# Performance work log

Hardware: AMD Instinct MI355X
Metric: run time of the kernel (lower is better)

Reference implementation:

```python
import jax, jax.numpy as jnp
import numpy as np

B, D, G, L = 8, 128, 2048, 24
GF = G // 2 + 1  # rfft bins
EPS = 1e-5


def setup_inputs() -> dict:
    key = jax.random.key(0)
    ks = jax.random.split(key, 6)
    x = jax.random.normal(ks[0], (B, D, G), dtype=jnp.float32)
    Phi_f = jax.random.normal(ks[1], (L, GF), dtype=jnp.float32) * 0.1
    Theta = jax.random.normal(ks[2], (L, D, D), dtype=jnp.float32) * (1.0 / np.sqrt(D))
    ln_gamma = jnp.ones((D,), dtype=jnp.float32)
    ln_beta = jnp.zeros((D,), dtype=jnp.float32)
    fc1_w = jax.random.normal(ks[3], (2 * D, D), dtype=jnp.float32) * (1.0 / np.sqrt(D))
    fc1_b = jnp.zeros((2 * D,), dtype=jnp.float32)
    fc2_w = jax.random.normal(ks[4], (D, 2 * D), dtype=jnp.float32) * (1.0 / np.sqrt(2 * D))
    fc2_b = jnp.zeros((D,), dtype=jnp.float32)
    return {
        'x': x, 'Phi_f': Phi_f, 'Theta': Theta,
        'ln_gamma': ln_gamma, 'ln_beta': ln_beta,
        'fc1_w': fc1_w, 'fc1_b': fc1_b, 'fc2_w': fc2_w, 'fc2_b': fc2_b,
    }


def reference(x, Phi_f, Theta, ln_gamma, ln_beta, fc1_w, fc1_b, fc2_w, fc2_b):
    # x: (B, D, G). LayerNorm over the lifting (channel) dim D.
    mean = jnp.mean(x, axis=1, keepdims=True)
    var = jnp.var(x, axis=1, keepdims=True)
    z = (x - mean) * jax.lax.rsqrt(var + EPS)
    z = z * ln_gamma[None, :, None] + ln_beta[None, :, None]

    # Spectral convolution with each Hilbert filter.
    Xf = jnp.fft.rfft(z, axis=-1)                       # (B, D, GF) complex
    Uf = Xf[:, :, None, :] * jnp.conj(Phi_f)[None, None]  # (B, D, L, GF)
    U = jnp.fft.irfft(Uf, n=G, axis=-1)                 # (B, D, L, G)

    # Per-filter channel mixing then reduction over filters:
    # einsum('bdln,lhd->bhln') followed by sum over l, fused:
    S = jnp.einsum('bdlg,lhd->bhg', U, Theta)           # (B, D, G)

    # Pointwise MLP (Conv1d kernel_size=1 == channel matmul).
    H = jnp.einsum('hd,bdg->bhg', fc1_w, S) + fc1_b[None, :, None]
    H = jax.nn.gelu(H, approximate=False)
    out = jnp.einsum('dh,bhg->bdg', fc2_w, H) + fc2_b[None, :, None]
    return x + out
```

## Files before the change

### kernel.cpp

```cpp
#include <hip/hip_runtime.h>
#include <math.h>


#define B_   8
#define D_   128
#define G_   2048
#define L_   24
#define GF_  1025
#define BD_  1024
#define DD_  16384
#define GH_  1024
#define CF_  1026
#define MF_  1088
#define NF_  2048

#define PA_CV0 64
#define PA_TT0 130
#define PA_WF0 386
#define PA_WI0 1474
#define PA_END 2498

#define G1_NB  544
#define G1_END 4768

typedef __attribute__((ext_vector_type(8))) short  short8v;
typedef __attribute__((ext_vector_type(4))) float  float4v;

union FU { float f; unsigned int u; };
union V8 { short8v v; ushort u[8]; };
union V4 { uint2 p; ushort u[4]; };

static __device__ __forceinline__ float bf2f(ushort h) {
    FU v; v.u = ((unsigned int)h) << 16; return v.f;
}
static __device__ __forceinline__ ushort f2bf(float f) {
    FU v; v.f = f;
    unsigned int r = v.u + 0x7fffu + ((v.u >> 16) & 1u);
    return (ushort)(r >> 16);
}
static __device__ __forceinline__ void async16(const void* g, void* l) {
    __builtin_amdgcn_global_load_lds(
        (const __attribute__((address_space(1))) void*)g,
        (__attribute__((address_space(3))) void*)l, 16, 0, 0);
}
static __device__ __forceinline__ int is_f32(const unsigned int* graw) {
    return graw[0] == 0x3F800000u;
}

__global__ __launch_bounds__(256) void k_pre(
        const void* __restrict__ x_raw,  const void* __restrict__ th_raw,
        const unsigned int* __restrict__ graw, const void* __restrict__ be_raw,
        const void* __restrict__ w1_raw, const void* __restrict__ b1_raw,
        const void* __restrict__ w2_raw, const void* __restrict__ b2_raw,
        ushort* __restrict__ z,  ushort* __restrict__ wf,
        ushort* __restrict__ wi, ushort* __restrict__ thT,
        ushort* __restrict__ w1c, ushort* __restrict__ b1c,
        ushort* __restrict__ w2c, ushort* __restrict__ b2c) {
    __shared__ ushort T[L_][72];
    int bid = blockIdx.x, tid = threadIdx.x;

    if (bid < PA_CV0) {
        int fl = is_f32(graw);
        int b  = bid >> 3;
        int g  = (bid & 7) * 256 + tid;
        float s = 0.f, ss = 0.f;
        if (fl) {
            const float* xp = (const float*)x_raw + (size_t)b * D_ * G_ + g;
            for (int d = 0; d < D_; ++d) {
                float v = xp[(size_t)d * G_];
                s += v; ss += v * v;
            }
        } else {
            const ushort* xp = (const ushort*)x_raw + (size_t)b * D_ * G_ + g;
            for (int d = 0; d < D_; ++d) {
                float v = bf2f(xp[(size_t)d * G_]);
                s += v; ss += v * v;
            }
        }
        float mean = s * (1.f / D_);
        float var  = ss * (1.f / D_) - mean * mean;
        float inv  = rsqrtf(var + 1e-5f);
        ushort* zp = z + (size_t)(g & 1) * (BD_ * GH_) +
                     (size_t)(b * D_) * GH_ + (g >> 1);
        if (fl) {
            const float* xp = (const float*)x_raw + (size_t)b * D_ * G_ + g;
            const float* gp = (const float*)graw;
            const float* bp = (const float*)be_raw;
            for (int d = 0; d < D_; ++d) {
                float o = (xp[(size_t)d * G_] - mean) * inv * gp[d] + bp[d];
                zp[(size_t)d * GH_] = f2bf(o);
            }
        } else {
            const ushort* xp = (const ushort*)x_raw + (size_t)b * D_ * G_ + g;
            const ushort* gp = (const ushort*)graw;
            const ushort* bp = (const ushort*)be_raw;
            for (int d = 0; d < D_; ++d) {
                float o = (bf2f(xp[(size_t)d * G_]) - mean) * inv * bf2f(gp[d])
                        + bf2f(bp[d]);
                zp[(size_t)d * GH_] = f2bf(o);
            }
        }
    } else if (bid < PA_TT0) {
        int fl = is_f32(graw);
        int lb = bid - PA_CV0;
        const void* src; ushort* dst; int n, rel;
        if (lb < 32)       { src = w1_raw; dst = w1c; n = 32768; rel = lb; }
        else if (lb == 32) { src = b1_raw; dst = b1c; n = 256;   rel = 0; }
        else if (lb < 65)  { src = w2_raw; dst = w2c; n = 32768; rel = lb - 33; }
        else               { src = b2_raw; dst = b2c; n = 128;   rel = 0; }
        int i0 = rel * 1024 + tid * 4;
        if (fl) {
            const float* s = (const float*)src;
            #pragma unroll
            for (int j = 0; j < 4; ++j) {
                int k = i0 + j;
                if (k < n) dst[k] = f2bf(s[k]);
            }
        } else {
            const ushort* s = (const ushort*)src;
            #pragma unroll
            for (int j = 0; j < 4; ++j) {
                int k = i0 + j;
                if (k < n) dst[k] = s[k];
            }
        }
    } else if (bid < PA_WF0) {
        int fl = is_f32(graw);
        int hd0 = (bid - PA_TT0) * 64;
        if (tid < 192) {
            int l = tid >> 3, c8 = tid & 7;
            V8 o;
            if (fl) {
                const float* tp = (const float*)th_raw + (size_t)l * DD_ +
                                  hd0 + c8 * 8;
                float4v a0 = *(const float4v*)tp;
                float4v a1 = *(const float4v*)(tp + 4);
                #pragma unroll
                for (int j = 0; j < 4; ++j) {
                    o.u[j] = f2bf(a0[j]); o.u[4 + j] = f2bf(a1[j]);
                }
            } else {
                o.v = *(const short8v*)((const ushort*)th_raw +
                                        (size_t)l * DD_ + hd0 + c8 * 8);
            }
            *(short8v*)&T[l][c8 * 8] = o.v;
        }
        __syncthreads();
        int hdl = tid & 63, part = tid >> 6;
        V8 o;
        #pragma unroll
        for (int j = 0; j < 8; ++j) {
            int l = part * 8 + j;
            o.u[j] = (l < L_) ? T[l][hdl] : (ushort)0;
        }
        *(short8v*)(thT + (size_t)(hd0 + hdl) * 32 + part * 8) = o.v;
    } else if (bid < PA_WI0) {
        int c  = bid - PA_WF0;
        int g0 = tid * 4;
        V4 v;
        if (c >= CF_) {
            #pragma unroll
            for (int j = 0; j < 4; ++j) v.u[j] = 0;
        } else {
            int f = c >> 1, im = c & 1;
            #pragma unroll
            for (int j = 0; j < 4; ++j) {
                int g = g0 + j;
                int r = (f * g) & (GH_ - 1);
                float th = (float)r * 6.135923151542565e-3f;
                v.u[j] = f2bf(im ? -__sinf(th) : __cosf(th));
            }
        }
        *(uint2*)(wf + (size_t)c * GH_ + g0) = v.p;
    } else {
        int g = bid - PA_WI0;
        for (int ch = tid; ch < MF_ / 8; ch += 256) {
            int c0 = ch * 8;
            V8 v;
            #pragma unroll
            for (int j = 0; j < 8; ++j) {
                int c = c0 + j;
                if (c >= CF_) { v.u[j] = 0; continue; }
                int f = c >> 1, im = c & 1;
                float a = (f == 0 || f == GH_ / 2) ? (1.f / 2048.f)
                                                   : (1.f / 1024.f);
                int r = (f * g) & (GH_ - 1);
                float th = (float)r * 6.135923151542565e-3f;
                v.u[j] = f2bf(im ? -a * __sinf(th) : a * __cosf(th));
            }
            *(short8v*)(wi + (size_t)g * MF_ + c0) = v.v;
        }
    }
}

__global__ __launch_bounds__(256, 4) void k_g1(
        const ushort* __restrict__ wf, const ushort* __restrict__ z,
        float* __restrict__ zft,
        const void* __restrict__ phi_raw, const unsigned int* __restrict__ graw,
        const ushort* __restrict__ thT, ushort* __restrict__ M) {
    __shared__ ushort As[2][64 * 64];
    __shared__ ushort Bs[2][64 * 64];
    __shared__ ushort Aph[16][40];
    int bid = blockIdx.x, tid = threadIdx.x;
    int w = tid >> 6, lane = tid & 63;
    int lr = lane & 15, q = lane >> 4;

    if (bid < G1_NB) {
        int m0 = (bid >> 5) * 64;
        int n0 = (bid & 31) * 64;
        int wm = (w & 1) * 32, wn = (w >> 1) * 32;
        int rl = lane >> 3, c8 = (lane & 7) ^ rl;
        int t0 = w * 2, t1 = w * 2 + 1;
        const ushort* gA0 = wf + (size_t)(m0 + t0 * 8 + rl) * GH_ + c8 * 8;
        const ushort* gA1 = wf + (size_t)(m0 + t1 * 8 + rl) * GH_ + c8 * 8;
        const ushort* gB0 = z  + (size_t)(n0 + t0 * 8 + rl) * GH_ + c8 * 8;
        const ushort* gB1 = z  + (size_t)(n0 + t1 * 8 + rl) * GH_ + c8 * 8;

        float4v acc00 = {0.f,0.f,0.f,0.f}, acc01 = {0.f,0.f,0.f,0.f};
        float4v acc10 = {0.f,0.f,0.f,0.f}, acc11 = {0.f,0.f,0.f,0.f};

        async16(gA0, &As[0][t0 * 512]);
        async16(gA1, &As[0][t1 * 512]);
        async16(gB0, &Bs[0][t0 * 512]);
        async16(gB1, &Bs[0][t1 * 512]);
        __syncthreads();

        int buf = 0;
        for (int k0 = 0; k0 < GH_; k0 += 64) {
            if (k0 + 64 < GH_) {
                int nb = buf ^ 1;
                async16(gA0 + k0 + 64, &As[nb][t0 * 512]);
                async16(gA1 + k0 + 64, &As[nb][t1 * 512]);
                async16(gB0 + k0 + 64, &Bs[nb][t0 * 512]);
                async16(gB1 + k0 + 64, &Bs[nb][t1 * 512]);
            }
            const ushort* Ab = &As[buf][0];
            const ushort* Bb = &Bs[buf][0];
            #pragma unroll
            for (int s = 0; s < 2; ++s) {
                int cs = s * 4 + q;
                int ra0 = wm + lr, ra1 = wm + 16 + lr;
                int rb0 = wn + lr, rb1 = wn + 16 + lr;
                short8v a0 = *(const short8v*)(Ab + ra0 * 64 + ((cs ^ (ra0 & 7)) << 3));
                short8v a1 = *(const short8v*)(Ab + ra1 * 64 + ((cs ^ (ra1 & 7)) << 3));
                short8v b0 = *(const short8v*)(Bb + rb0 * 64 + ((cs ^ (rb0 & 7)) << 3));
                short8v b1 = *(const short8v*)(Bb + rb1 * 64 + ((cs ^ (rb1 & 7)) << 3));
                acc00 = __builtin_amdgcn_mfma_f32_16x16x32_bf16(a0, b0, acc00, 0, 0, 0);
                acc01 = __builtin_amdgcn_mfma_f32_16x16x32_bf16(a0, b1, acc01, 0, 0, 0);
                acc10 = __builtin_amdgcn_mfma_f32_16x16x32_bf16(a1, b0, acc10, 0, 0, 0);
                acc11 = __builtin_amdgcn_mfma_f32_16x16x32_bf16(a1, b1, acc11, 0, 0, 0);
            }
            __syncthreads();
            buf ^= 1;
        }

        float4v accs[2][2] = { { acc00, acc01 }, { acc10, acc11 } };
        #pragma unroll
        for (int i = 0; i < 2; ++i)
            #pragma unroll
            for (int j = 0; j < 2; ++j) {
                int col = n0 + wn + j * 16 + lr;
                int row = m0 + wm + i * 16 + q * 4;
                #pragma unroll
                for (int r = 0; r < 4; ++r)
                    zft[(size_t)(row + r) * NF_ + col] = accs[i][j][r];
            }
    } else {
        int bb  = bid - G1_NB;
        int f0  = (bb >> 6) * 16;
        int hd0 = (bb & 63) * 256;
        int isf = is_f32(graw);
        #pragma unroll
        for (int rep = 0; rep < 2; ++rep) {
            int idx = rep * 256 + tid;
            int fl = idx >> 5, l = idx & 31;
            int f = f0 + fl;
            ushort v = 0;
            if (l < L_ && f < GF_)
                v = isf ? f2bf(((const float*)phi_raw)[(size_t)l * GF_ + f])
                        : ((const ushort*)phi_raw)[(size_t)l * GF_ + f];
            Aph[fl][l] = v;
        }
        __syncthreads();
        short8v a = *(const short8v*)&Aph[lr][q * 8];
        #pragma unroll
        for (int t = 0; t < 4; ++t) {
            int n = hd0 + (w * 4 + t) * 16 + lr;
            short8v b = *(const short8v*)(thT + (size_t)n * 32 + q * 8);
            float4v c = {0.f, 0.f, 0.f, 0.f};
            c = __builtin_amdgcn_mfma_f32_16x16x32_bf16(a, b, c, 0, 0, 0);
            #pragma unroll
            for (int r = 0; r < 4; ++r) {
                int f = f0 + q * 4 + r;
                if (f < GF_) M[(size_t)f * DD_ + n] = f2bf(c[r]);
            }
        }
    }
}

__global__ __launch_bounds__(256, 2) void k_mix3(const float* __restrict__ zft,
                                                 const ushort* __restrict__ M,
                                                 ushort* __restrict__ sft) {
    int fp  = blockIdx.x;
    int fb  = GH_ - fp;
    int tid = threadIdx.x;
    int w = tid >> 6, lane = tid & 63;
    int lr = lane & 15, q = lane >> 4;
    int cc = lr >> 3, bb = lr & 7;

    float ang = (float)fp * 3.0679615757712823e-3f;
    float wr  = cosf(ang), sn = sinf(ang);
    float wi_ = -sn;
    float wsig = cc ? wi_ : -wi_;
    float cbv  = cc ? wr  : -wr;
    float asgn = cc ? -1.f : 1.f;

    const float* rc = zft + (size_t)(2 * fp + cc) * NF_;
    const float* ro = zft + (size_t)(2 * fp + (cc ^ 1)) * NF_;
    int colb = bb * 128 + q * 8;

    short8v aZ[4], aZb[4];
    #pragma unroll
    for (int s = 0; s < 4; ++s) {
        int col = colb + s * 32;
        float4v av0 = *(const float4v*)(rc + col);
        float4v av1 = *(const float4v*)(rc + col + 4);
        float4v bv0 = *(const float4v*)(rc + BD_ + col);
        float4v bv1 = *(const float4v*)(rc + BD_ + col + 4);
        float4v bo0 = *(const float4v*)(ro + BD_ + col);
        float4v bo1 = *(const float4v*)(ro + BD_ + col + 4);
        V8 tz, tb;
        #pragma unroll
        for (int j = 0; j < 4; ++j) {
            float av = av0[j], bv = bv0[j], bo = bo0[j];
            float zz = fmaf(wsig, bo, fmaf(wr, bv, av));
            float zb = fmaf(cbv, bv, fmaf(wi_, bo, asgn * av));
            tz.u[j] = f2bf(zz); tb.u[j] = f2bf(zb);
            av = av1[j]; bv = bv1[j]; bo = bo1[j];
            zz = fmaf(wsig, bo, fmaf(wr, bv, av));
            zb = fmaf(cbv, bv, fmaf(wi_, bo, asgn * av));
            tz.u[4 + j] = f2bf(zz); tb.u[4 + j] = f2bf(zb);
        }
        aZ[s] = tz.v; aZb[s] = tb.v;
    }

    const ushort* Mf = M + (size_t)fp * DD_;
    const ushort* Mb = M + (size_t)fb * DD_;
    #pragma unroll
    for (int n = 0; n < 2; ++n) {
        int nt = 2 * w + n;
        float4v c1 = {0.f, 0.f, 0.f, 0.f};
        float4v c2 = {0.f, 0.f, 0.f, 0.f};
        #pragma unroll
        for (int s = 0; s < 4; ++s) {
            short8v b1 = *(const short8v*)(Mf + (size_t)(nt * 16 + lr) * D_ +
                                           s * 32 + q * 8);
            short8v b2 = *(const short8v*)(Mb + (size_t)(nt * 16 + lr) * D_ +
                                           s * 32 + q * 8);
            c1 = __builtin_amdgcn_mfma_f32_16x16x32_bf16(aZ[s],  b1, c1, 0, 0, 0);
            c2 = __builtin_amdgcn_mfma_f32_16x16x32_bf16(aZb[s], b2, c2, 0, 0, 0);
        }
        #pragma unroll
        for (int r = 0; r < 4; ++r) {
            int p   = q * 4 + r;
            int c2i = p >> 3, b2 = p & 7;
            float sgm = c2i ? -1.f : 1.f;
            float se  = c1[r] + sgm * c2[r];
            float sop = c1[r] - sgm * c2[r];
            float pp  = __shfl_xor(sop, 32);
            float tsg = c2i ? sn : -sn;
            float so  = fmaf(tsg, pp, sop * wr);
            size_t rowo = (size_t)(2 * fp + c2i) * NF_;
            int colh = b2 * 128 + nt * 16 + lr;
            sft[rowo + colh]       = f2bf(se);
            sft[rowo + BD_ + colh] = f2bf(so);
        }
    }
}

__global__ __launch_bounds__(256, 4) void k_gemm64t(const ushort* __restrict__ A,
                                                    const ushort* __restrict__ Bm,
                                                    float* __restrict__ C,
                                                    int K, int lda, int ldb,
                                                    int ldc, int kv) {
    __shared__ ushort As[2][64 * 64];
    __shared__ ushort Bs[2][64 * 64];
    int tid = threadIdx.x;
    int m0 = blockIdx.x * 64, n0 = blockIdx.y * 64;
    int w = tid >> 6, lane = tid & 63;
    int lr = lane & 15, q = lane >> 4;
    int wm = (w & 1) * 32, wn = (w >> 1) * 32;

    int rl = lane >> 3, c8 = (lane & 7) ^ rl;
    int t0 = w * 2, t1 = w * 2 + 1;
    const ushort* gA0 = A + (size_t)(m0 + t0 * 8 + rl) * lda + c8 * 8;
    const ushort* gA1 = A + (size_t)(m0 + t1 * 8 + rl) * lda + c8 * 8;

    int br = tid >> 2;
    int bc = tid & 3;

    float4v acc00 = {0.f,0.f,0.f,0.f}, acc01 = {0.f,0.f,0.f,0.f};
    float4v acc10 = {0.f,0.f,0.f,0.f}, acc11 = {0.f,0.f,0.f,0.f};

    async16(gA0, &As[0][t0 * 512]);
    async16(gA1, &As[0][t1 * 512]);
    {
        V8 u0, u1;
        if (br < kv) {
            const ushort* gb = Bm + (size_t)br * ldb + n0 + bc * 16;
            u0.v = *(const short8v*)gb;
            u1.v = *(const short8v*)(gb + 8);
        } else {
            #pragma unroll
            for (int j = 0; j < 8; ++j) { u0.u[j] = 0; u1.u[j] = 0; }
        }
        #pragma unroll
        for (int j = 0; j < 8; ++j) {
            int n = bc * 16 + j;
            Bs[0][n * 64 + ((((br >> 3) ^ (n & 7)) << 3) | (br & 7))] = u0.u[j];
        }
        #pragma unroll
        for (int j = 0; j < 8; ++j) {
            int n = bc * 16 + 8 + j;
            Bs[0][n * 64 + ((((br >> 3) ^ (n & 7)) << 3) | (br & 7))] = u1.u[j];
        }
    }
    __syncthreads();

    int buf = 0;
    for (int k0 = 0; k0 < K; k0 += 64) {
        V8 u0, u1;
        bool more = (k0 + 64 < K);
        if (more) {
            int nb = buf ^ 1;
            async16(gA0 + k0 + 64, &As[nb][t0 * 512]);
            async16(gA1 + k0 + 64, &As[nb][t1 * 512]);
            int kr = k0 + 64 + br;
            if (kr < kv) {
                const ushort* gb = Bm + (size_t)kr * ldb + n0 + bc * 16;
                u0.v = *(const short8v*)gb;
                u1.v = *(const short8v*)(gb + 8);
            } else {
                #pragma unroll
                for (int j = 0; j < 8; ++j) { u0.u[j] = 0; u1.u[j] = 0; }
            }
        }
        const ushort* Ab = &As[buf][0];
        const ushort* Bb = &Bs[buf][0];
        #pragma unroll
        for (int s = 0; s < 2; ++s) {
            int cs = s * 4 + q;
            int ra0 = wm + lr, ra1 = wm + 16 + lr;
            int rb0 = wn + lr, rb1 = wn + 16 + lr;
            short8v a0 = *(const short8v*)(Ab + ra0 * 64 + ((cs ^ (ra0 & 7)) << 3));
            short8v a1 = *(const short8v*)(Ab + ra1 * 64 + ((cs ^ (ra1 & 7)) << 3));
            short8v b0 = *(const short8v*)(Bb + rb0 * 64 + ((cs ^ (rb0 & 7)) << 3));
            short8v b1 = *(const short8v*)(Bb + rb1 * 64 + ((cs ^ (rb1 & 7)) << 3));
            acc00 = __builtin_amdgcn_mfma_f32_16x16x32_bf16(a0, b0, acc00, 0, 0, 0);
            acc01 = __builtin_amdgcn_mfma_f32_16x16x32_bf16(a0, b1, acc01, 0, 0, 0);
            acc10 = __builtin_amdgcn_mfma_f32_16x16x32_bf16(a1, b0, acc10, 0, 0, 0);
            acc11 = __builtin_amdgcn_mfma_f32_16x16x32_bf16(a1, b1, acc11, 0, 0, 0);
        }
        __syncthreads();
        if (more) {
            int nb = buf ^ 1;
            #pragma unroll
            for (int j = 0; j < 8; ++j) {
                int n = bc * 16 + j;
                Bs[nb][n * 64 + ((((br >> 3) ^ (n & 7)) << 3) | (br & 7))] = u0.u[j];
            }
            #pragma unroll
            for (int j = 0; j < 8; ++j) {
                int n = bc * 16 + 8 + j;
                Bs[nb][n * 64 + ((((br >> 3) ^ (n & 7)) << 3) | (br & 7))] = u1.u[j];
            }
        }
        __syncthreads();
        buf ^= 1;
    }

    float4v accs[2][2] = { { acc00, acc01 }, { acc10, acc11 } };
    #pragma unroll
    for (int i = 0; i < 2; ++i)
        #pragma unroll
        for (int j = 0; j < 2; ++j) {
            int col = n0 + wn + j * 16 + lr;
            int row = m0 + wm + i * 16 + q * 4;
            #pragma unroll
            for (int r = 0; r < 4; ++r)
                C[(size_t)(row + r) * ldc + col] = accs[i][j][r];
        }
}

#define MLPG 32
__global__ __launch_bounds__(256, 2) void k_mlp3(const float* __restrict__ ST,
                                                 const void* __restrict__ x0,
                                                 const ushort* __restrict__ w1,
                                                 const ushort* __restrict__ b1,
                                                 const ushort* __restrict__ w2,
                                                 const ushort* __restrict__ b2,
                                                 const unsigned int* __restrict__ graw,
                                                 void* __restrict__ outv) {
    __shared__ ushort Sb[MLPG][136];
    __shared__ ushort Hb[MLPG][264];
    __shared__ float  Ob[128][36];
    int g0 = blockIdx.x * MLPG, b = blockIdx.y;
    int tid = threadIdx.x;
    {
        int col = tid >> 3, seg = tid & 7;
        int g = g0 + col;
        const float* sp = ST + (size_t)(g >> 1) * NF_ + (g & 1) * BD_ +
                          b * D_ + seg * 16;
        float4v v0 = *(const float4v*)(sp);
        float4v v1 = *(const float4v*)(sp + 4);
        float4v v2 = *(const float4v*)(sp + 8);
        float4v v3 = *(const float4v*)(sp + 12);
        V8 o0, o1;
        #pragma unroll
        for (int k = 0; k < 4; ++k) { o0.u[k] = f2bf(v0[k]); o0.u[4 + k] = f2bf(v1[k]); }
        #pragma unroll
        for (int k = 0; k < 4; ++k) { o1.u[k] = f2bf(v2[k]); o1.u[4 + k] = f2bf(v3[k]); }
        *(short8v*)&Sb[col][seg * 16]     = o0.v;
        *(short8v*)&Sb[col][seg * 16 + 8] = o1.v;
    }
    __syncthreads();
    int w = tid >> 6, lane = tid & 63;
    int lr = lane & 15, q = lane >> 4;
    int nt = w & 1, mh = w >> 1;

    {
        float4v acc[8];
        #pragma unroll
        for (int i = 0; i < 8; ++i) { float4v zz = {0.f,0.f,0.f,0.f}; acc[i] = zz; }
        #pragma unroll
        for (int ks = 0; ks < 4; ++ks) {
            short8v bf = *(const short8v*)&Sb[nt * 16 + lr][ks * 32 + q * 8];
            #pragma unroll
            for (int i = 0; i < 8; ++i) {
                int mt = mh * 8 + i;
                short8v af = *(const short8v*)(w1 + (size_t)(mt * 16 + lr) * D_ +
                                               ks * 32 + q * 8);
                acc[i] = __builtin_amdgcn_mfma_f32_16x16x32_bf16(af, bf, acc[i], 0, 0, 0);
            }
        }
        #pragma unroll
        for (int i = 0; i < 8; ++i) {
            int h0 = (mh * 8 + i) * 16 + q * 4;
            V4 hv;
            #pragma unroll
            for (int r = 0; r < 4; ++r) {
                float v = acc[i][r] + bf2f(b1[h0 + r]);
                v = 0.5f * v * (1.f + erff(v * 0.70710678118f));
                hv.u[r] = f2bf(v);
            }
            *(uint2*)&Hb[nt * 16 + lr][h0] = hv.p;
        }
    }
    __syncthreads();
    {
        float4v acc2[4];
        #pragma unroll
        for (int j = 0; j < 4; ++j) { float4v zz = {0.f,0.f,0.f,0.f}; acc2[j] = zz; }
        #pragma unroll
        for (int ks = 0; ks < 8; ++ks) {
            short8v bf = *(const short8v*)&Hb[nt * 16 + lr][ks * 32 + q * 8];
            #pragma unroll
            for (int j = 0; j < 4; ++j) {
                int mt2 = mh * 4 + j;
                short8v af = *(const short8v*)(w2 + (size_t)(mt2 * 16 + lr) * (2 * D_) +
                                               ks * 32 + q * 8);
                acc2[j] = __builtin_amdgcn_mfma_f32_16x16x32_bf16(af, bf, acc2[j], 0, 0, 0);
            }
        }
        int col = nt * 16 + lr;
        #pragma unroll
        for (int j = 0; j < 4; ++j) {
            int d0 = (mh * 4 + j) * 16 + q * 4;
            #pragma unroll
            for (int r = 0; r < 4; ++r)
                Ob[d0 + r][col] = acc2[j][r] + bf2f(b2[d0 + r]);
        }
    }
    __syncthreads();
    {
        int fl = is_f32(graw);
        if (fl) {
            #pragma unroll
            for (int p = 0; p < 4; ++p) {
                int idx = p * 256 + tid;
                int d = idx >> 3, c4 = (idx & 7) * 4;
                float4v o = *(const float4v*)&Ob[d][c4];
                size_t gidx = ((size_t)(b * D_ + d)) * G_ + g0 + c4;
                float4v xv = *(const float4v*)((const float*)x0 + gidx);
                float4v ov;
                #pragma unroll
                for (int k = 0; k < 4; ++k) ov[k] = o[k] + xv[k];
                *(float4v*)((float*)outv + gidx) = ov;
            }
        } else {
            #pragma unroll
            for (int p = 0; p < 4; ++p) {
                int idx = p * 256 + tid;
                int d = idx >> 3, c4 = (idx & 7) * 4;
                float4v o = *(const float4v*)&Ob[d][c4];
                size_t gidx = ((size_t)(b * D_ + d)) * G_ + g0 + c4;
                V4 xv; xv.p = *(const uint2*)((const ushort*)x0 + gidx);
                V4 ov;
                #pragma unroll
                for (int k = 0; k < 4; ++k) ov.u[k] = f2bf(o[k] + bf2f(xv.u[k]));
                *(uint2*)((ushort*)outv + gidx) = ov.p;
            }
        }
    }
}

extern "C" void kernel_launch(void* const* d_in, const int* in_sizes, int n_in,
                              void* d_out, int out_size, void* d_ws, size_t ws_size,
                              hipStream_t stream) {
    char* base = (char*)d_ws;
    ushort* z    = (ushort*)(base);
    ushort* wf   = (ushort*)(base + 4194304);
    ushort* sft  = (ushort*)(base);
    float*  zft  = (float*)(base + 13107200);
    float*  st   = (float*)(base + 13107200);
    ushort* w1c  = (ushort*)(base + 27050048);
    ushort* b1c  = (ushort*)(base + 27115584);
    ushort* w2c  = (ushort*)(base + 27116096);
    ushort* b2c  = (ushort*)(base + 27181632);
    ushort* Mm   = (ushort*)(base + 27182592);
    ushort* wi   = (ushort*)(base + 60769792);
    ushort* thT  = (ushort*)(base + 69420544);

    const unsigned int* graw = (const unsigned int*)d_in[3];

    k_pre    <<<dim3(PA_END), 256, 0, stream>>>(
        d_in[0], d_in[2], graw, d_in[4], d_in[5], d_in[6], d_in[7], d_in[8],
        z, wf, wi, thT, w1c, b1c, w2c, b2c);
    k_g1     <<<dim3(G1_END), 256, 0, stream>>>(wf, z, zft, d_in[1], graw,
                                                thT, Mm);
    k_mix3   <<<dim3(513), 256, 0, stream>>>(zft, Mm, sft);
    k_gemm64t<<<dim3(GH_ / 64, NF_ / 64), 256, 0, stream>>>(
        wi, sft, st, MF_, MF_, NF_, NF_, CF_);
    k_mlp3   <<<dim3(G_ / MLPG, B_), 256, 0, stream>>>(st, d_in[0], w1c, b1c,
                                                       w2c, b2c, graw, d_out);
}
```

Baseline: 168.8 us.

## Widen forward-DFT GEMM tile, split LayerNorm over channels, emit bf16 spectral output

The forward DFT GEMM in k_g1 moves from 64x64 to 128x64 tiles, with each wave computing a 64x32 sub-tile. This raises MFMA work per LDS B-fragment load and cuts the block count. The M dimension is padded to 1152 rows, with launch bounds reduced to 3 waves per SIMD. The LayerNorm pre-pass now splits each column's 128 channels across four waves, reduces the statistics in LDS and keeps x in registers, so there are more blocks and no second global read of x. The inverse-DFT GEMM writes bf16 instead of fp32 and the MLP reads it directly, halving that intermediate's traffic at a small precision cost.

```diff
diff --git a/kernel.cpp b/kernel.cpp
--- a/kernel.cpp
+++ b/kernel.cpp
@@ -12,16 +12,17 @@
 #define GH_  1024
 #define CF_  1026
 #define MF_  1088
+#define MFW_ 1152
 #define NF_  2048
 
-#define PA_CV0 64
-#define PA_TT0 130
-#define PA_WF0 386
-#define PA_WI0 1474
-#define PA_END 2498
-
-#define G1_NB  544
-#define G1_END 4768
+#define PA_CV0 256
+#define PA_TT0 322
+#define PA_WF0 578
+#define PA_WI0 1730
+#define PA_END 2754
+
+#define G1_NB  288
+#define G1_END 4512
 
 typedef __attribute__((ext_vector_type(8))) short  short8v;
 typedef __attribute__((ext_vector_type(4))) float  float4v;
@@ -57,46 +58,64 @@
         ushort* __restrict__ w1c, ushort* __restrict__ b1c,
         ushort* __restrict__ w2c, ushort* __restrict__ b2c) {
     __shared__ ushort T[L_][72];
+    __shared__ float red[2][256];
+    __shared__ float mi[2][64];
     int bid = blockIdx.x, tid = threadIdx.x;
 
     if (bid < PA_CV0) {
         int fl = is_f32(graw);
-        int b  = bid >> 3;
-        int g  = (bid & 7) * 256 + tid;
+        int b  = bid >> 5;
+        int g0 = (bid & 31) * 64;
+        int gi = tid & 63, dq = tid >> 6;
+        int g  = g0 + gi;
+        int d0 = dq * 32;
+        float vals[32];
         float s = 0.f, ss = 0.f;
         if (fl) {
-            const float* xp = (const float*)x_raw + (size_t)b * D_ * G_ + g;
-            for (int d = 0; d < D_; ++d) {
+            const float* xp = (const float*)x_raw + (size_t)(b * D_ + d0) * G_ + g;
+            #pragma unroll 8
+            for (int d = 0; d < 32; ++d) {
                 float v = xp[(size_t)d * G_];
-                s += v; ss += v * v;
+                vals[d] = v; s += v; ss += v * v;
             }
         } else {
-            const ushort* xp = (const ushort*)x_raw + (size_t)b * D_ * G_ + g;
-            for (int d = 0; d < D_; ++d) {
+            const ushort* xp = (const ushort*)x_raw + (size_t)(b * D_ + d0) * G_ + g;
+            #pragma unroll 8
+            for (int d = 0; d < 32; ++d) {
                 float v = bf2f(xp[(size_t)d * G_]);
-                s += v; ss += v * v;
-            }
-        }
-        float mean = s * (1.f / D_);
-        float var  = ss * (1.f / D_) - mean * mean;
-        float inv  = rsqrtf(var + 1e-5f);
+                vals[d] = v; s += v; ss += v * v;
+            }
+        }
+        red[0][tid] = s; red[1][tid] = ss;
+        __syncthreads();
+        if (tid < 64) {
+            float S  = red[0][tid] + red[0][tid + 64] + red[0][tid + 128] +
+                       red[0][tid + 192];
+            float SS = red[1][tid] + red[1][tid + 64] + red[1][tid + 128] +
+                       red[1][tid + 192];
+            float mean = S * (1.f / D_);
+            float var  = SS * (1.f / D_) - mean * mean;
+            mi[0][tid] = mean;
+            mi[1][tid] = rsqrtf(var + 1e-5f);
+        }
+        __syncthreads();
+        float mean = mi[0][gi], inv = mi[1][gi];
         ushort* zp = z + (size_t)(g & 1) * (BD_ * GH_) +
-                     (size_t)(b * D_) * GH_ + (g >> 1);
+                     (size_t)(b * D_ + d0) * GH_ + (g >> 1);
         if (fl) {
-            const float* xp = (const float*)x_raw + (size_t)b * D_ * G_ + g;
-            const float* gp = (const float*)graw;
-            const float* bp = (const float*)be_raw;
-            for (int d = 0; d < D_; ++d) {
-                float o = (xp[(size_t)d * G_] - mean) * inv * gp[d] + bp[d];
+            const float* gp = (const float*)graw + d0;
+            const float* bp = (const float*)be_raw + d0;
+            #pragma unroll 8
+            for (int d = 0; d < 32; ++d) {
+                float o = (vals[d] - mean) * inv * gp[d] + bp[d];
                 zp[(size_t)d * GH_] = f2bf(o);
             }
         } else {
-            const ushort* xp = (const ushort*)x_raw + (size_t)b * D_ * G_ + g;
-            const ushort* gp = (const ushort*)graw;
-            const ushort* bp = (const ushort*)be_raw;
-            for (int d = 0; d < D_; ++d) {
-                float o = (bf2f(xp[(size_t)d * G_]) - mean) * inv * bf2f(gp[d])
-                        + bf2f(bp[d]);
+            const ushort* gp = (const ushort*)graw + d0;
+            const ushort* bp = (const ushort*)be_raw + d0;
+            #pragma unroll 8
+            for (int d = 0; d < 32; ++d) {
+                float o = (vals[d] - mean) * inv * bf2f(gp[d]) + bf2f(bp[d]);
                 zp[(size_t)d * GH_] = f2bf(o);
             }
         }
@@ -193,12 +212,12 @@
     }
 }
 
-__global__ __launch_bounds__(256, 4) void k_g1(
+__global__ __launch_bounds__(256, 3) void k_g1(
         const ushort* __restrict__ wf, const ushort* __restrict__ z,
         float* __restrict__ zft,
         const void* __restrict__ phi_raw, const unsigned int* __restrict__ graw,
         const ushort* __restrict__ thT, ushort* __restrict__ M) {
-    __shared__ ushort As[2][64 * 64];
+    __shared__ ushort As[2][128 * 64];
     __shared__ ushort Bs[2][64 * 64];
     __shared__ ushort Aph[16][40];
     int bid = blockIdx.x, tid = threadIdx.x;
@@ -206,64 +225,74 @@
     int lr = lane & 15, q = lane >> 4;
 
     if (bid < G1_NB) {
-        int m0 = (bid >> 5) * 64;
+        int m0 = (bid >> 5) * 128;
         int n0 = (bid & 31) * 64;
-        int wm = (w & 1) * 32, wn = (w >> 1) * 32;
+        int wm = (w & 1) * 64, wn = (w >> 1) * 32;
         int rl = lane >> 3, c8 = (lane & 7) ^ rl;
-        int t0 = w * 2, t1 = w * 2 + 1;
-        const ushort* gA0 = wf + (size_t)(m0 + t0 * 8 + rl) * GH_ + c8 * 8;
-        const ushort* gA1 = wf + (size_t)(m0 + t1 * 8 + rl) * GH_ + c8 * 8;
-        const ushort* gB0 = z  + (size_t)(n0 + t0 * 8 + rl) * GH_ + c8 * 8;
-        const ushort* gB1 = z  + (size_t)(n0 + t1 * 8 + rl) * GH_ + c8 * 8;
-
-        float4v acc00 = {0.f,0.f,0.f,0.f}, acc01 = {0.f,0.f,0.f,0.f};
-        float4v acc10 = {0.f,0.f,0.f,0.f}, acc11 = {0.f,0.f,0.f,0.f};
-
-        async16(gA0, &As[0][t0 * 512]);
-        async16(gA1, &As[0][t1 * 512]);
-        async16(gB0, &Bs[0][t0 * 512]);
-        async16(gB1, &Bs[0][t1 * 512]);
+        int ta = w * 4, tb = w * 2;
+        const ushort* gA0 = wf + (size_t)(m0 + (ta    ) * 8 + rl) * GH_ + c8 * 8;
+        const ushort* gA1 = wf + (size_t)(m0 + (ta + 1) * 8 + rl) * GH_ + c8 * 8;
+        const ushort* gA2 = wf + (size_t)(m0 + (ta + 2) * 8 + rl) * GH_ + c8 * 8;
+        const ushort* gA3 = wf + (size_t)(m0 + (ta + 3) * 8 + rl) * GH_ + c8 * 8;
+        const ushort* gB0 = z  + (size_t)(n0 + (tb    ) * 8 + rl) * GH_ + c8 * 8;
+        const ushort* gB1 = z  + (size_t)(n0 + (tb + 1) * 8 + rl) * GH_ + c8 * 8;
+
+        float4v acc[4][2];
+        #pragma unroll
+        for (int i = 0; i < 4; ++i)
+            #pragma unroll
+            for (int j = 0; j < 2; ++j) {
+                float4v zz = {0.f, 0.f, 0.f, 0.f}; acc[i][j] = zz;
+            }
+
+        async16(gA0, &As[0][(ta    ) * 512]);
+        async16(gA1, &As[0][(ta + 1) * 512]);
+        async16(gA2, &As[0][(ta + 2) * 512]);
+        async16(gA3, &As[0][(ta + 3) * 512]);
+        async16(gB0, &Bs[0][(tb    ) * 512]);
+        async16(gB1, &Bs[0][(tb + 1) * 512]);
         __syncthreads();
 
         int buf = 0;
         for (int k0 = 0; k0 < GH_; k0 += 64) {
             if (k0 + 64 < GH_) {
                 int nb = buf ^ 1;
-                async16(gA0 + k0 + 64, &As[nb][t0 * 512]);
-                async16(gA1 + k0 + 64, &As[nb][t1 * 512]);
-                async16(gB0 + k0 + 64, &Bs[nb][t0 * 512]);
-                async16(gB1 + k0 + 64, &Bs[nb][t1 * 512]);
+                async16(gA0 + k0 + 64, &As[nb][(ta    ) * 512]);
+                async16(gA1 + k0 + 64, &As[nb][(ta + 1) * 512]);
+                async16(gA2 + k0 + 64, &As[nb][(ta + 2) * 512]);
+                async16(gA3 + k0 + 64, &As[nb][(ta + 3) * 512]);
+                async16(gB0 + k0 + 64, &Bs[nb][(tb    ) * 512]);
+                async16(gB1 + k0 + 64, &Bs[nb][(tb + 1) * 512]);
             }
             const ushort* Ab = &As[buf][0];
             const ushort* Bb = &Bs[buf][0];
             #pragma unroll
             for (int s = 0; s < 2; ++s) {
                 int cs = s * 4 + q;
-                int ra0 = wm + lr, ra1 = wm + 16 + lr;
                 int rb0 = wn + lr, rb1 = wn + 16 + lr;
-                short8v a0 = *(const short8v*)(Ab + ra0 * 64 + ((cs ^ (ra0 & 7)) << 3));
-                short8v a1 = *(const short8v*)(Ab + ra1 * 64 + ((cs ^ (ra1 & 7)) << 3));
                 short8v b0 = *(const short8v*)(Bb + rb0 * 64 + ((cs ^ (rb0 & 7)) << 3));
                 short8v b1 = *(const short8v*)(Bb + rb1 * 64 + ((cs ^ (rb1 & 7)) << 3));
-                acc00 = __builtin_amdgcn_mfma_f32_16x16x32_bf16(a0, b0, acc00, 0, 0, 0);
-                acc01 = __builtin_amdgcn_mfma_f32_16x16x32_bf16(a0, b1, acc01, 0, 0, 0);
-                acc10 = __builtin_amdgcn_mfma_f32_16x16x32_bf16(a1, b0, acc10, 0, 0, 0);
-                acc11 = __builtin_amdgcn_mfma_f32_16x16x32_bf16(a1, b1, acc11, 0, 0, 0);
+                #pragma unroll
+                for (int i = 0; i < 4; ++i) {
+                    int ra = wm + i * 16 + lr;
+                    short8v a = *(const short8v*)(Ab + ra * 64 + ((cs ^ (ra & 7)) << 3));
+                    acc[i][0] = __builtin_amdgcn_mfma_f32_16x16x32_bf16(a, b0, acc[i][0], 0, 0, 0);
+                    acc[i][1] = __builtin_amdgcn_mfma_f32_16x16x32_bf16(a, b1, acc[i][1], 0, 0, 0);
+                }
             }
             __syncthreads();
             buf ^= 1;
         }
 
-        float4v accs[2][2] = { { acc00, acc01 }, { acc10, acc11 } };
-        #pragma unroll
-        for (int i = 0; i < 2; ++i)
+        #pragma unroll
+        for (int i = 0; i < 4; ++i)
             #pragma unroll
             for (int j = 0; j < 2; ++j) {
                 int col = n0 + wn + j * 16 + lr;
                 int row = m0 + wm + i * 16 + q * 4;
                 #pragma unroll
                 for (int r = 0; r < 4; ++r)
-                    zft[(size_t)(row + r) * NF_ + col] = accs[i][j][r];
+                    zft[(size_t)(row + r) * NF_ + col] = acc[i][j][r];
             }
     } else {
         int bb  = bid - G1_NB;
@@ -380,7 +409,7 @@
 
 __global__ __launch_bounds__(256, 4) void k_gemm64t(const ushort* __restrict__ A,
                                                     const ushort* __restrict__ Bm,
-                                                    float* __restrict__ C,
+                                                    ushort* __restrict__ C,
                                                     int K, int lda, int ldb,
                                                     int ldc, int kv) {
     __shared__ ushort As[2][64 * 64];
@@ -488,12 +517,12 @@
             int row = m0 + wm + i * 16 + q * 4;
             #pragma unroll
             for (int r = 0; r < 4; ++r)
-                C[(size_t)(row + r) * ldc + col] = accs[i][j][r];
+                C[(size_t)(row + r) * ldc + col] = f2bf(accs[i][j][r]);
         }
 }
 
 #define MLPG 32
-__global__ __launch_bounds__(256, 2) void k_mlp3(const float* __restrict__ ST,
+__global__ __launch_bounds__(256, 2) void k_mlp3(const ushort* __restrict__ ST,
                                                  const void* __restrict__ x0,
                                                  const ushort* __restrict__ w1,
                                                  const ushort* __restrict__ b1,
@@ -509,19 +538,12 @@
     {
         int col = tid >> 3, seg = tid & 7;
         int g = g0 + col;
-        const float* sp = ST + (size_t)(g >> 1) * NF_ + (g & 1) * BD_ +
-                          b * D_ + seg * 16;
-        float4v v0 = *(const float4v*)(sp);
-        float4v v1 = *(const float4v*)(sp + 4);
-        float4v v2 = *(const float4v*)(sp + 8);
-        float4v v3 = *(const float4v*)(sp + 12);
-        V8 o0, o1;
-        #pragma unroll
-        for (int k = 0; k < 4; ++k) { o0.u[k] = f2bf(v0[k]); o0.u[4 + k] = f2bf(v1[k]); }
-        #pragma unroll
-        for (int k = 0; k < 4; ++k) { o1.u[k] = f2bf(v2[k]); o1.u[4 + k] = f2bf(v3[k]); }
-        *(short8v*)&Sb[col][seg * 16]     = o0.v;
-        *(short8v*)&Sb[col][seg * 16 + 8] = o1.v;
+        const ushort* sp = ST + (size_t)(g >> 1) * NF_ + (g & 1) * BD_ +
+                           b * D_ + seg * 16;
+        short8v s0 = *(const short8v*)(sp);
+        short8v s1 = *(const short8v*)(sp + 8);
+        *(short8v*)&Sb[col][seg * 16]     = s0;
+        *(short8v*)&Sb[col][seg * 16 + 8] = s1;
     }
     __syncthreads();
     int w = tid >> 6, lane = tid & 63;
@@ -622,7 +644,7 @@
     ushort* wf   = (ushort*)(base + 4194304);
     ushort* sft  = (ushort*)(base);
     float*  zft  = (float*)(base + 13107200);
-    float*  st   = (float*)(base + 13107200);
+    ushort* st   = (ushort*)(base + 13107200);
     ushort* w1c  = (ushort*)(base + 27050048);
     ushort* b1c  = (ushort*)(base + 27115584);
     ushort* w2c  = (ushort*)(base + 27116096);
```

Measured after the change: 166.9 us. No clear change (-1.1%).
